# Performance work log

Hardware: AMD Instinct MI355X
Metric: run time of the kernel (lower is better)

Reference implementation:

```python
import jax, jax.numpy as jnp
import numpy as np

N_NODES = 100000
N_EDGES = 1600000
DIM = 64
N_GRAPHS = 1000


def setup_inputs() -> dict:
    key = jax.random.key(0)
    ks = jax.random.split(key, 6)
    s = 1.0 / np.sqrt(DIM)
    x = jax.random.normal(ks[0], (N_NODES, DIM), dtype=jnp.float32)
    edge_index = jax.random.randint(ks[1], (2, N_EDGES), 0, N_NODES, dtype=jnp.int64)
    batch = jnp.sort(jax.random.randint(ks[2], (N_NODES,), 0, N_GRAPHS, dtype=jnp.int64))
    W1 = jax.random.normal(ks[3], (DIM, DIM), dtype=jnp.float32) * s
    b1 = jnp.zeros((DIM,), jnp.float32)
    W2 = jax.random.normal(ks[4], (DIM, DIM), dtype=jnp.float32) * s
    b2 = jnp.zeros((DIM,), jnp.float32)
    return {"x": x, "W1": W1, "b1": b1, "W2": W2, "b2": b2,
            "edge_index": edge_index, "batch": batch}


def reference(x, W1, b1, W2, b2, edge_index, batch):
    n = x.shape[0]
    loop = jnp.arange(n, dtype=edge_index.dtype)
    src = jnp.concatenate([edge_index[0], loop])  # [E+N] with self-loops
    dst = jnp.concatenate([edge_index[1], loop])
    # symmetric GCN normalization: deg^{-1/2}[src] * deg^{-1/2}[dst]
    deg = jax.ops.segment_sum(jnp.ones(src.shape[0], x.dtype), dst, num_segments=n)
    dinv = jax.lax.rsqrt(jnp.maximum(deg, 1.0))  # deg >= 1 due to self-loops
    norm = (dinv[src] * dinv[dst])[:, None]      # [E+N, 1]

    def gcn(h, W, b):
        h = h @ W                                  # transform first (smaller dim path)
        msg = h[src] * norm                        # gather + normalize
        return jax.ops.segment_sum(msg, dst, num_segments=n) + b

    h = jax.nn.relu(gcn(x, W1, b1))
    # dropout: eval mode -> identity
    h = jax.nn.relu(gcn(h, W2, b2))

    counts = jax.ops.segment_sum(jnp.ones((n,), x.dtype), batch, num_segments=N_GRAPHS)
    pooled = jax.ops.segment_sum(h, batch, num_segments=N_GRAPHS)
    return pooled / jnp.maximum(counts, 1.0)[:, None]
```

## Files before the change

kernel.cpp:

```cpp
#include <hip/hip_runtime.h>
#include <hip/hip_fp16.h>

#define DIM 64
#define BIN_SHIFT 7
#define BINSZ 128
#define MAXBINS 1024
#define PB 512
#define PB_LOG 9

typedef __attribute__((ext_vector_type(2))) float floatx2;


__global__ __launch_bounds__(256) void k_hist(const int* __restrict__ dst,
                                              int* __restrict__ C, int E, int NB) {
    __shared__ int h[MAXBINS];
    for (int i = threadIdx.x; i < NB; i += 256) h[i] = 0;
    __syncthreads();
    int per = (E + PB - 1) / PB;
    int e0 = blockIdx.x * per;
    int e1 = e0 + per; if (e1 > E) e1 = E;
    for (int e = e0 + (int)threadIdx.x; e < e1; e += 256)
        atomicAdd(&h[dst[e] >> BIN_SHIFT], 1);
    __syncthreads();
    for (int i = threadIdx.x; i < NB; i += 256)
        C[blockIdx.x * NB + i] = h[i];
}


__global__ __launch_bounds__(1024) void k_scanA(const int* __restrict__ C,
                                                int* __restrict__ S,
                                                int* __restrict__ bsums, int NB, int M) {
    __shared__ int sh[1024];
    int tid = threadIdx.x;
    int j0 = blockIdx.x * 4096 + tid * 4;
    int v[4]; int sum = 0;
#pragma unroll
    for (int t = 0; t < 4; ++t) {
        int j = j0 + t; int x = 0;
        if (j < M) { int bin = j >> PB_LOG, blk = j & (PB - 1); x = C[blk * NB + bin]; }
        v[t] = sum; sum += x;
    }
    sh[tid] = sum;
    __syncthreads();
#pragma unroll
    for (int d = 1; d < 1024; d <<= 1) {
        int t = (tid >= d) ? sh[tid - d] : 0;
        __syncthreads();
        sh[tid] += t;
        __syncthreads();
    }
    int excl = sh[tid] - sum;
#pragma unroll
    for (int t = 0; t < 4; ++t) {
        int j = j0 + t;
        if (j < M) S[j] = excl + v[t];
    }
    if (tid == 1023) bsums[blockIdx.x] = sh[1023];
}


__global__ __launch_bounds__(1024) void k_scanB(int* __restrict__ bsums, int nb) {
    __shared__ int s[1024];
    int tid = threadIdx.x;
    int v = (tid < nb) ? bsums[tid] : 0;
    s[tid] = v;
    __syncthreads();
#pragma unroll
    for (int d = 1; d < 1024; d <<= 1) {
        int t = (tid >= d) ? s[tid - d] : 0;
        __syncthreads();
        s[tid] += t;
        __syncthreads();
    }
    if (tid < nb) bsums[tid] = s[tid] - v;
}


__global__ __launch_bounds__(256) void k_bucket(const int* __restrict__ src,
                                                const int* __restrict__ dst,
                                                const int* __restrict__ S,
                                                const int* __restrict__ bsums,
                                                int* __restrict__ bkt, int E, int NB) {
    __shared__ int lcur[MAXBINS];
    int blk = blockIdx.x;
    for (int i = threadIdx.x; i < NB; i += 256) {
        int j = i * PB + blk;
        lcur[i] = S[j] + bsums[j >> 12];
    }
    __syncthreads();
    int per = (E + PB - 1) / PB;
    int e0 = blk * per;
    int e1 = e0 + per; if (e1 > E) e1 = E;
    for (int e = e0 + (int)threadIdx.x; e < e1; e += 256) {
        int d = dst[e];
        int pos = atomicAdd(&lcur[d >> BIN_SHIFT], 1);
        bkt[pos] = src[e] | ((d & (BINSZ - 1)) << 24);
    }
}


__global__ __launch_bounds__(256) void k_binsort(const int* __restrict__ bkt,
                                                 const int* __restrict__ S,
                                                 const int* __restrict__ bsums,
                                                 int* __restrict__ csr,
                                                 int* __restrict__ off,
                                                 float* __restrict__ dinv,
                                                 const int* __restrict__ batch,
                                                 int* __restrict__ goff,
                                                 int N, int G, int E, int NB) {
    __shared__ int cnt[BINSZ], bas[BINSZ], cur[BINSZ];
    __shared__ int wsum[4];
    int tid = threadIdx.x;
    int b = blockIdx.x;
    int j0 = b << PB_LOG;
    int s0 = S[j0] + bsums[j0 >> 12];
    int s1 = E;
    if (b + 1 < NB) { int j1 = (b + 1) << PB_LOG; s1 = S[j1] + bsums[j1 >> 12]; }
    if (tid < BINSZ) { cnt[tid] = 0; cur[tid] = 0; }
    __syncthreads();
    for (int i = s0 + tid; i < s1; i += 256)
        atomicAdd(&cnt[(bkt[i] >> 24) & (BINSZ - 1)], 1);
    __syncthreads();
    int my = (tid < BINSZ) ? cnt[tid] : 0;
    int lane = tid & 63, wv = tid >> 6;
    int x = my;
#pragma unroll
    for (int d = 1; d < 64; d <<= 1) {
        int t = __shfl_up(x, d);
        if (lane >= d) x += t;
    }
    if (lane == 63) wsum[wv] = x;
    __syncthreads();
    int prefix = 0;
    for (int w = 0; w < wv; ++w) prefix += wsum[w];
    int ex = x + prefix - my;
    if (tid < BINSZ) {
        bas[tid] = ex;
        int v = (b << BIN_SHIFT) + tid;
        if (v < N) {
            off[v] = s0 + ex;
            dinv[v] = rsqrtf((float)(my + 1));
            if (v == N - 1) off[N] = E;
            int bb = batch[v];
            int prev = (v == 0) ? -1 : batch[v - 1];
            for (int g = prev + 1; g <= bb; ++g) goff[g] = v;
            if (v == N - 1)
                for (int g = bb + 1; g <= G; ++g) goff[g] = N;
        }
    }
    __syncthreads();
    for (int i = s0 + tid; i < s1; i += 256) {
        int p = bkt[i];
        int lo = (p >> 24) & (BINSZ - 1);
        int li = atomicAdd(&cur[lo], 1);
        csr[s0 + bas[lo] + li] = p & 0xFFFFFF;
    }
}


__global__ __launch_bounds__(256) void k_gemm(const float* __restrict__ Xf,
                                              const __half* __restrict__ Xh,
                                              const float* __restrict__ W,
                                              const float* __restrict__ dinv,
                                              __half* __restrict__ Y, int N,
                                              int relu_in, int fp8out) {
    __shared__ float Ws[64 * 64];
    __shared__ float Xs[16 * 64];
    int tid = threadIdx.x;
#pragma unroll
    for (int i = 0; i < 16; ++i) Ws[tid + 256 * i] = W[tid + 256 * i];

    int row0 = blockIdx.x * 16;
    int r = tid >> 4, c4 = (tid & 15) << 2;
    int row = row0 + r;
    {
        float4 v = make_float4(0.f, 0.f, 0.f, 0.f);
        if (row < N) {
            if (Xh) {
                uint2 u = *(const uint2*)(Xh + (size_t)row * DIM + c4);
                float2 f0 = __half22float2(*(__half2*)&u.x);
                float2 f1 = __half22float2(*(__half2*)&u.y);
                v = make_float4(f0.x, f0.y, f1.x, f1.y);
            } else {
                v = *(const float4*)(Xf + (size_t)row * DIM + c4);
            }
            if (relu_in) {
                v.x = fmaxf(v.x, 0.f); v.y = fmaxf(v.y, 0.f);
                v.z = fmaxf(v.z, 0.f); v.w = fmaxf(v.w, 0.f);
            }
        }
        *(float4*)(Xs + r * DIM + c4) = v;
    }
    __syncthreads();

    float4 acc = make_float4(0.f, 0.f, 0.f, 0.f);
#pragma unroll
    for (int k = 0; k < 64; ++k) {
        float xk = Xs[r * DIM + k];
        float4 w = *(const float4*)(Ws + k * DIM + c4);
        acc.x += xk * w.x; acc.y += xk * w.y;
        acc.z += xk * w.z; acc.w += xk * w.w;
    }
    if (fp8out) {
        unsigned int* Y8 = (unsigned int*)Y;
        if (row < N) {
            float s = dinv[row];
            int p = 0;
            p = __builtin_amdgcn_cvt_pk_fp8_f32(acc.x * s, acc.y * s, p, false);
            p = __builtin_amdgcn_cvt_pk_fp8_f32(acc.z * s, acc.w * s, p, true);
            Y8[(size_t)row * 16 + (c4 >> 2)] = (unsigned int)p;
        } else if (row == N) {
            Y8[(size_t)row * 16 + (c4 >> 2)] = 0u;
        }
    } else {
        if (row < N) {
            float s = dinv[row];
            __half2 p0 = __floats2half2_rn(acc.x * s, acc.y * s);
            __half2 p1 = __floats2half2_rn(acc.z * s, acc.w * s);
            uint2 u;
            u.x = *(unsigned int*)&p0;
            u.y = *(unsigned int*)&p1;
            *(uint2*)(Y + (size_t)row * DIM + c4) = u;
        } else if (row == N) {
            uint2 z; z.x = 0u; z.y = 0u;
            *(uint2*)(Y + (size_t)row * DIM + c4) = z;
        }
    }
}


__device__ __forceinline__ float4 gather_rows(const unsigned int* __restrict__ hs8,
                                              const int* __restrict__ csr,
                                              int k0, int k1, int v, int l, int gw4,
                                              int N) {
    float4 accA, accB;
    {
        unsigned int u = hs8[(size_t)v * 16 + l];
        floatx2 f0 = __builtin_amdgcn_cvt_pk_f32_fp8((int)u, false);
        floatx2 f1 = __builtin_amdgcn_cvt_pk_f32_fp8((int)u, true);
        accA = make_float4(f0.x, f0.y, f1.x, f1.y);
        accB = make_float4(0.f, 0.f, 0.f, 0.f);
    }
    for (int kb = k0; kb < k1; kb += 16) {
        int rem = k1 - kb;
        int idx = N;
        if (l < rem) idx = csr[kb + l];
        int mm = rem < 16 ? rem : 16;
        for (int j = 0; j < mm; j += 4) {
            int sA = __shfl(idx, gw4 + j);
            int sB = __shfl(idx, gw4 + j + 1);
            int sC = __shfl(idx, gw4 + j + 2);
            int sD = __shfl(idx, gw4 + j + 3);
            unsigned int uA = hs8[(size_t)sA * 16 + l];
            unsigned int uB = hs8[(size_t)sB * 16 + l];
            unsigned int uC = hs8[(size_t)sC * 16 + l];
            unsigned int uD = hs8[(size_t)sD * 16 + l];
            floatx2 pA0 = __builtin_amdgcn_cvt_pk_f32_fp8((int)uA, false);
            floatx2 pA1 = __builtin_amdgcn_cvt_pk_f32_fp8((int)uA, true);
            floatx2 pB0 = __builtin_amdgcn_cvt_pk_f32_fp8((int)uB, false);
            floatx2 pB1 = __builtin_amdgcn_cvt_pk_f32_fp8((int)uB, true);
            floatx2 pC0 = __builtin_amdgcn_cvt_pk_f32_fp8((int)uC, false);
            floatx2 pC1 = __builtin_amdgcn_cvt_pk_f32_fp8((int)uC, true);
            floatx2 pD0 = __builtin_amdgcn_cvt_pk_f32_fp8((int)uD, false);
            floatx2 pD1 = __builtin_amdgcn_cvt_pk_f32_fp8((int)uD, true);
            accA.x += pA0.x + pB0.x; accA.y += pA0.y + pB0.y;
            accA.z += pA1.x + pB1.x; accA.w += pA1.y + pB1.y;
            accB.x += pC0.x + pD0.x; accB.y += pC0.y + pD0.y;
            accB.z += pC1.x + pD1.x; accB.w += pC1.y + pD1.y;
        }
    }
    return make_float4(accA.x + accB.x, accA.y + accB.y,
                       accA.z + accB.z, accA.w + accB.w);
}


__global__ __launch_bounds__(256) void k_gather_gemm(const unsigned int* __restrict__ hs8,
                                                     const int* __restrict__ csr,
                                                     const int* __restrict__ off,
                                                     const float* __restrict__ dinv,
                                                     const float* __restrict__ bias,
                                                     const float* __restrict__ W,
                                                     unsigned int* __restrict__ hs_out,
                                                     int N) {
    __shared__ float Ws[64 * 64];
    __shared__ float Xs[16 * 64];
    int tid = threadIdx.x;
#pragma unroll
    for (int i = 0; i < 16; ++i) Ws[tid + 256 * i] = W[tid + 256 * i];
    if (blockIdx.x == 0 && tid < 16)
        hs_out[(size_t)N * 16 + tid] = 0u;

    int r = tid >> 4;
    int l = tid & 15;
    int gw4 = ((tid >> 4) & 3) << 4;
    int v = blockIdx.x * 16 + r;

    float dv = 0.f;
    float4 h = make_float4(0.f, 0.f, 0.f, 0.f);
    if (v < N) {
        dv = dinv[v];
        float4 bv = ((const float4*)bias)[l];
        float4 acc = gather_rows(hs8, csr, off[v], off[v + 1], v, l, gw4, N);
        h.x = fmaxf(acc.x * dv + bv.x, 0.f);
        h.y = fmaxf(acc.y * dv + bv.y, 0.f);
        h.z = fmaxf(acc.z * dv + bv.z, 0.f);
        h.w = fmaxf(acc.w * dv + bv.w, 0.f);
    }
    *(float4*)(Xs + r * DIM + (l << 2)) = h;
    __syncthreads();

    float4 o = make_float4(0.f, 0.f, 0.f, 0.f);
#pragma unroll
    for (int k = 0; k < 64; ++k) {
        float xk = Xs[r * DIM + k];
        float4 w = *(const float4*)(Ws + k * DIM + (l << 2));
        o.x += xk * w.x; o.y += xk * w.y;
        o.z += xk * w.z; o.w += xk * w.w;
    }
    if (v < N) {
        int p = 0;
        p = __builtin_amdgcn_cvt_pk_fp8_f32(o.x * dv, o.y * dv, p, false);
        p = __builtin_amdgcn_cvt_pk_fp8_f32(o.z * dv, o.w * dv, p, true);
        hs_out[(size_t)v * 16 + l] = (unsigned int)p;
    }
}


__global__ __launch_bounds__(256) void k_gather16(const unsigned int* __restrict__ hs8,
                                                  const int* __restrict__ csr,
                                                  const int* __restrict__ off,
                                                  const float* __restrict__ dinv,
                                                  const float* __restrict__ bias,
                                                  __half* __restrict__ agg, int N) {
    int tid = threadIdx.x;
    int v = blockIdx.x * 16 + (tid >> 4);
    if (v >= N) return;
    int l = tid & 15;
    int gw4 = ((tid >> 4) & 3) << 4;
    float dv = dinv[v];
    float4 bv = ((const float4*)bias)[l];
    float4 acc = gather_rows(hs8, csr, off[v], off[v + 1], v, l, gw4, N);
    __half2 p0 = __floats2half2_rn(acc.x * dv + bv.x, acc.y * dv + bv.y);
    __half2 p1 = __floats2half2_rn(acc.z * dv + bv.z, acc.w * dv + bv.w);
    uint2 u;
    u.x = *(unsigned int*)&p0;
    u.y = *(unsigned int*)&p1;
    ((uint2*)(agg + (size_t)v * DIM))[l] = u;
}


__global__ __launch_bounds__(256) void k_pool(const __half* __restrict__ agg,
                                              const int* __restrict__ goff,
                                              float* __restrict__ out, int G) {
    int g = blockIdx.x * 4 + (threadIdx.x >> 6);
    if (g >= G) return;
    int lane = threadIdx.x & 63;
    int q = lane >> 4, c = lane & 15;
    const uint2* h2 = (const uint2*)agg;
    int n0 = goff[g], n1 = goff[g + 1];
    float4 acc = make_float4(0.f, 0.f, 0.f, 0.f);
    for (int i = n0 + q; i < n1; i += 4) {
        uint2 u = h2[(size_t)i * 16 + c];
        float2 f0 = __half22float2(*(__half2*)&u.x);
        float2 f1 = __half22float2(*(__half2*)&u.y);
        acc.x += fmaxf(f0.x, 0.f); acc.y += fmaxf(f0.y, 0.f);
        acc.z += fmaxf(f1.x, 0.f); acc.w += fmaxf(f1.y, 0.f);
    }
    acc.x += __shfl_down(acc.x, 32); acc.y += __shfl_down(acc.y, 32);
    acc.z += __shfl_down(acc.z, 32); acc.w += __shfl_down(acc.w, 32);
    acc.x += __shfl_down(acc.x, 16); acc.y += __shfl_down(acc.y, 16);
    acc.z += __shfl_down(acc.z, 16); acc.w += __shfl_down(acc.w, 16);
    if (q == 0) {
        float inv = 1.0f / fmaxf((float)(n1 - n0), 1.0f);
        *(float4*)(out + ((size_t)g << 6) + (c << 2)) =
            make_float4(acc.x * inv, acc.y * inv, acc.z * inv, acc.w * inv);
    }
}


static inline int cdiv(int a, int b) { return (a + b - 1) / b; }

extern "C" void kernel_launch(void* const* d_in, const int* in_sizes, int n_in,
                              void* d_out, int out_size, void* d_ws, size_t ws_size,
                              hipStream_t stream) {
    const float* x   = (const float*)d_in[0];
    const float* W1  = (const float*)d_in[1];
    const float* b1  = (const float*)d_in[2];
    const float* W2  = (const float*)d_in[3];
    const float* b2  = (const float*)d_in[4];
    const int*   ei  = (const int*)d_in[5];
    const int*   bat = (const int*)d_in[6];

    const int N = in_sizes[0] / DIM;
    const int E = in_sizes[5] / 2;
    const int G = out_size / DIM;
    const int NB = cdiv(N, BINSZ);
    const int M  = NB * PB;
    const int* src = ei;
    const int* dst = ei + E;
    float* out = (float*)d_out;

    __half* hs1    = (__half*)d_ws;
    __half* hs2    = hs1 + (size_t)(N + 1) * DIM;
    __half* agg1   = hs2 + (size_t)(N + 1) * DIM;
    float*  dinv   = (float*)(agg1 + (size_t)N * DIM);
    int*    off    = (int*)(dinv + N);
    int*    goff   = off + (N + 1);
    int*    C      = goff + (G + 1);
    int*    S      = C + (size_t)PB * NB;
    int*    bsums  = S + (size_t)PB * NB;
    int*    csr    = bsums + 1024;
    int*    bkt    = (int*)hs1;
    __half* agg2   = hs1;

    k_hist<<<PB, 256, 0, stream>>>(dst, C, E, NB);
    int nb2 = cdiv(M, 4096);
    k_scanA<<<nb2, 1024, 0, stream>>>(C, S, bsums, NB, M);
    k_scanB<<<1, 1024, 0, stream>>>(bsums, nb2);
    k_bucket<<<PB, 256, 0, stream>>>(src, dst, S, bsums, bkt, E, NB);
    k_binsort<<<NB, 256, 0, stream>>>(bkt, S, bsums, csr, off, dinv, bat, goff, N, G, E, NB);

    k_gemm<<<cdiv(N + 1, 16), 256, 0, stream>>>(x, nullptr, W1, dinv, hs1, N, 0, 1);

    k_gather_gemm<<<cdiv(N, 16), 256, 0, stream>>>((const unsigned int*)hs1, csr, off,
                                                   dinv, b1, W2, (unsigned int*)hs2, N);

    k_gather16<<<cdiv(N, 16), 256, 0, stream>>>((const unsigned int*)hs2, csr, off,
                                                dinv, b2, agg2, N);

    k_pool<<<cdiv(G, 4), 256, 0, stream>>>(agg2, goff, out, G);
}
```

Before: 226.7 us.

## Sort nodes by degree within bins to balance gather waves; widen unroll

The binsort kernel now computes, within each 128-node bin, a rank of every node by in-degree and writes a permutation array. The gather kernels take their node from this permutation, so the 16-lane groups sharing a wavefront have similar edge counts and lose less time to divergence. The gather inner loop is unrolled to 8 neighbor loads with four accumulators and 32-bit index math, and the unused fp16 paths of the gemm kernel are removed. The cost is an O(128) rank loop per thread in binsort, an extra indirection per node, and scattered output writes.

```diff
diff --git a/kernel.cpp b/kernel.cpp
--- a/kernel.cpp
+++ b/kernel.cpp
@@ -107,6 +107,7 @@
                                                  float* __restrict__ dinv,
                                                  const int* __restrict__ batch,
                                                  int* __restrict__ goff,
+                                                 int* __restrict__ nperm,
                                                  int N, int G, int E, int NB) {
     __shared__ int cnt[BINSZ], bas[BINSZ], cur[BINSZ];
     __shared__ int wsum[4];
@@ -148,6 +149,21 @@
                 for (int g = bb + 1; g <= G; ++g) goff[g] = N;
         }
     }
+    if (tid < BINSZ) {
+        int v = (b << BIN_SHIFT) + tid;
+        if (v < N) {
+            int nvalid = N - (b << BIN_SHIFT);
+            if (nvalid > BINSZ) nvalid = BINSZ;
+            int d = my, rk = 0;
+            for (int j = 0; j < nvalid; ++j) {
+                int dj = cnt[j];
+                rk += (int)((dj < d) || (dj == d && j < tid));
+            }
+            nperm[(b << BIN_SHIFT) + rk] = v;
+        } else {
+            nperm[v] = N;
+        }
+    }
     __syncthreads();
     for (int i = s0 + tid; i < s1; i += 256) {
         int p = bkt[i];
@@ -159,11 +175,9 @@
 
 
 __global__ __launch_bounds__(256) void k_gemm(const float* __restrict__ Xf,
-                                              const __half* __restrict__ Xh,
                                               const float* __restrict__ W,
                                               const float* __restrict__ dinv,
-                                              __half* __restrict__ Y, int N,
-                                              int relu_in, int fp8out) {
+                                              unsigned int* __restrict__ Y8, int N) {
     __shared__ float Ws[64 * 64];
     __shared__ float Xs[16 * 64];
     int tid = threadIdx.x;
@@ -175,20 +189,7 @@
     int row = row0 + r;
     {
         float4 v = make_float4(0.f, 0.f, 0.f, 0.f);
-        if (row < N) {
-            if (Xh) {
-                uint2 u = *(const uint2*)(Xh + (size_t)row * DIM + c4);
-                float2 f0 = __half22float2(*(__half2*)&u.x);
-                float2 f1 = __half22float2(*(__half2*)&u.y);
-                v = make_float4(f0.x, f0.y, f1.x, f1.y);
-            } else {
-                v = *(const float4*)(Xf + (size_t)row * DIM + c4);
-            }
-            if (relu_in) {
-                v.x = fmaxf(v.x, 0.f); v.y = fmaxf(v.y, 0.f);
-                v.z = fmaxf(v.z, 0.f); v.w = fmaxf(v.w, 0.f);
-            }
-        }
+        if (row < N) v = *(const float4*)(Xf + (size_t)row * DIM + c4);
         *(float4*)(Xs + r * DIM + c4) = v;
     }
     __syncthreads();
@@ -201,30 +202,14 @@
         acc.x += xk * w.x; acc.y += xk * w.y;
         acc.z += xk * w.z; acc.w += xk * w.w;
     }
-    if (fp8out) {
-        unsigned int* Y8 = (unsigned int*)Y;
-        if (row < N) {
-            float s = dinv[row];
-            int p = 0;
-            p = __builtin_amdgcn_cvt_pk_fp8_f32(acc.x * s, acc.y * s, p, false);
-            p = __builtin_amdgcn_cvt_pk_fp8_f32(acc.z * s, acc.w * s, p, true);
-            Y8[(size_t)row * 16 + (c4 >> 2)] = (unsigned int)p;
-        } else if (row == N) {
-            Y8[(size_t)row * 16 + (c4 >> 2)] = 0u;
-        }
-    } else {
-        if (row < N) {
-            float s = dinv[row];
-            __half2 p0 = __floats2half2_rn(acc.x * s, acc.y * s);
-            __half2 p1 = __floats2half2_rn(acc.z * s, acc.w * s);
-            uint2 u;
-            u.x = *(unsigned int*)&p0;
-            u.y = *(unsigned int*)&p1;
-            *(uint2*)(Y + (size_t)row * DIM + c4) = u;
-        } else if (row == N) {
-            uint2 z; z.x = 0u; z.y = 0u;
-            *(uint2*)(Y + (size_t)row * DIM + c4) = z;
-        }
+    if (row < N) {
+        float s = dinv[row];
+        int p = 0;
+        p = __builtin_amdgcn_cvt_pk_fp8_f32(acc.x * s, acc.y * s, p, false);
+        p = __builtin_amdgcn_cvt_pk_fp8_f32(acc.z * s, acc.w * s, p, true);
+        Y8[(size_t)row * 16 + (c4 >> 2)] = (unsigned int)p;
+    } else if (row == N) {
+        Y8[(size_t)row * 16 + (c4 >> 2)] = 0u;
     }
 }
 
@@ -233,50 +218,74 @@
                                               const int* __restrict__ csr,
                                               int k0, int k1, int v, int l, int gw4,
                                               int N) {
-    float4 accA, accB;
+    float4 a0, a1, a2, a3;
     {
-        unsigned int u = hs8[(size_t)v * 16 + l];
+        unsigned int u = hs8[(unsigned)((v << 4) | l)];
         floatx2 f0 = __builtin_amdgcn_cvt_pk_f32_fp8((int)u, false);
         floatx2 f1 = __builtin_amdgcn_cvt_pk_f32_fp8((int)u, true);
-        accA = make_float4(f0.x, f0.y, f1.x, f1.y);
-        accB = make_float4(0.f, 0.f, 0.f, 0.f);
+        a0 = make_float4(f0.x, f0.y, f1.x, f1.y);
+        a1 = make_float4(0.f, 0.f, 0.f, 0.f);
+        a2 = make_float4(0.f, 0.f, 0.f, 0.f);
+        a3 = make_float4(0.f, 0.f, 0.f, 0.f);
     }
     for (int kb = k0; kb < k1; kb += 16) {
         int rem = k1 - kb;
-        int idx = N;
-        if (l < rem) idx = csr[kb + l];
+        int idx = (l < rem) ? csr[kb + l] : N;
         int mm = rem < 16 ? rem : 16;
-        for (int j = 0; j < mm; j += 4) {
-            int sA = __shfl(idx, gw4 + j);
-            int sB = __shfl(idx, gw4 + j + 1);
-            int sC = __shfl(idx, gw4 + j + 2);
-            int sD = __shfl(idx, gw4 + j + 3);
-            unsigned int uA = hs8[(size_t)sA * 16 + l];
-            unsigned int uB = hs8[(size_t)sB * 16 + l];
-            unsigned int uC = hs8[(size_t)sC * 16 + l];
-            unsigned int uD = hs8[(size_t)sD * 16 + l];
-            floatx2 pA0 = __builtin_amdgcn_cvt_pk_f32_fp8((int)uA, false);
-            floatx2 pA1 = __builtin_amdgcn_cvt_pk_f32_fp8((int)uA, true);
-            floatx2 pB0 = __builtin_amdgcn_cvt_pk_f32_fp8((int)uB, false);
-            floatx2 pB1 = __builtin_amdgcn_cvt_pk_f32_fp8((int)uB, true);
-            floatx2 pC0 = __builtin_amdgcn_cvt_pk_f32_fp8((int)uC, false);
-            floatx2 pC1 = __builtin_amdgcn_cvt_pk_f32_fp8((int)uC, true);
-            floatx2 pD0 = __builtin_amdgcn_cvt_pk_f32_fp8((int)uD, false);
-            floatx2 pD1 = __builtin_amdgcn_cvt_pk_f32_fp8((int)uD, true);
-            accA.x += pA0.x + pB0.x; accA.y += pA0.y + pB0.y;
-            accA.z += pA1.x + pB1.x; accA.w += pA1.y + pB1.y;
-            accB.x += pC0.x + pD0.x; accB.y += pC0.y + pD0.y;
-            accB.z += pC1.x + pD1.x; accB.w += pC1.y + pD1.y;
+        for (int j = 0; j < mm; j += 8) {
+            int s0 = __shfl(idx, gw4 + j + 0);
+            int s1 = __shfl(idx, gw4 + j + 1);
+            int s2 = __shfl(idx, gw4 + j + 2);
+            int s3 = __shfl(idx, gw4 + j + 3);
+            int s4 = __shfl(idx, gw4 + j + 4);
+            int s5 = __shfl(idx, gw4 + j + 5);
+            int s6 = __shfl(idx, gw4 + j + 6);
+            int s7 = __shfl(idx, gw4 + j + 7);
+            unsigned int u0 = hs8[(unsigned)((s0 << 4) | l)];
+            unsigned int u1 = hs8[(unsigned)((s1 << 4) | l)];
+            unsigned int u2 = hs8[(unsigned)((s2 << 4) | l)];
+            unsigned int u3 = hs8[(unsigned)((s3 << 4) | l)];
+            unsigned int u4 = hs8[(unsigned)((s4 << 4) | l)];
+            unsigned int u5 = hs8[(unsigned)((s5 << 4) | l)];
+            unsigned int u6 = hs8[(unsigned)((s6 << 4) | l)];
+            unsigned int u7 = hs8[(unsigned)((s7 << 4) | l)];
+            floatx2 p0l = __builtin_amdgcn_cvt_pk_f32_fp8((int)u0, false);
+            floatx2 p0h = __builtin_amdgcn_cvt_pk_f32_fp8((int)u0, true);
+            floatx2 p1l = __builtin_amdgcn_cvt_pk_f32_fp8((int)u1, false);
+            floatx2 p1h = __builtin_amdgcn_cvt_pk_f32_fp8((int)u1, true);
+            floatx2 p2l = __builtin_amdgcn_cvt_pk_f32_fp8((int)u2, false);
+            floatx2 p2h = __builtin_amdgcn_cvt_pk_f32_fp8((int)u2, true);
+            floatx2 p3l = __builtin_amdgcn_cvt_pk_f32_fp8((int)u3, false);
+            floatx2 p3h = __builtin_amdgcn_cvt_pk_f32_fp8((int)u3, true);
+            floatx2 p4l = __builtin_amdgcn_cvt_pk_f32_fp8((int)u4, false);
+            floatx2 p4h = __builtin_amdgcn_cvt_pk_f32_fp8((int)u4, true);
+            floatx2 p5l = __builtin_amdgcn_cvt_pk_f32_fp8((int)u5, false);
+            floatx2 p5h = __builtin_amdgcn_cvt_pk_f32_fp8((int)u5, true);
+            floatx2 p6l = __builtin_amdgcn_cvt_pk_f32_fp8((int)u6, false);
+            floatx2 p6h = __builtin_amdgcn_cvt_pk_f32_fp8((int)u6, true);
+            floatx2 p7l = __builtin_amdgcn_cvt_pk_f32_fp8((int)u7, false);
+            floatx2 p7h = __builtin_amdgcn_cvt_pk_f32_fp8((int)u7, true);
+            a0.x += p0l.x; a0.y += p0l.y; a0.z += p0h.x; a0.w += p0h.y;
+            a1.x += p1l.x; a1.y += p1l.y; a1.z += p1h.x; a1.w += p1h.y;
+            a2.x += p2l.x; a2.y += p2l.y; a2.z += p2h.x; a2.w += p2h.y;
+            a3.x += p3l.x; a3.y += p3l.y; a3.z += p3h.x; a3.w += p3h.y;
+            a0.x += p4l.x; a0.y += p4l.y; a0.z += p4h.x; a0.w += p4h.y;
+            a1.x += p5l.x; a1.y += p5l.y; a1.z += p5h.x; a1.w += p5h.y;
+            a2.x += p6l.x; a2.y += p6l.y; a2.z += p6h.x; a2.w += p6h.y;
+            a3.x += p7l.x; a3.y += p7l.y; a3.z += p7h.x; a3.w += p7h.y;
         }
     }
-    return make_float4(accA.x + accB.x, accA.y + accB.y,
-                       accA.z + accB.z, accA.w + accB.w);
+    return make_float4(a0.x + a1.x + a2.x + a3.x,
+                       a0.y + a1.y + a2.y + a3.y,
+                       a0.z + a1.z + a2.z + a3.z,
+                       a0.w + a1.w + a2.w + a3.w);
 }
 
 
 __global__ __launch_bounds__(256) void k_gather_gemm(const unsigned int* __restrict__ hs8,
                                                      const int* __restrict__ csr,
                                                      const int* __restrict__ off,
+                                                     const int* __restrict__ nperm,
                                                      const float* __restrict__ dinv,
                                                      const float* __restrict__ bias,
                                                      const float* __restrict__ W,
@@ -293,7 +302,7 @@
     int r = tid >> 4;
     int l = tid & 15;
     int gw4 = ((tid >> 4) & 3) << 4;
-    int v = blockIdx.x * 16 + r;
+    int v = nperm[blockIdx.x * 16 + r];
 
     float dv = 0.f;
     float4 h = make_float4(0.f, 0.f, 0.f, 0.f);
@@ -329,11 +338,12 @@
 __global__ __launch_bounds__(256) void k_gather16(const unsigned int* __restrict__ hs8,
                                                   const int* __restrict__ csr,
                                                   const int* __restrict__ off,
+                                                  const int* __restrict__ nperm,
                                                   const float* __restrict__ dinv,
                                                   const float* __restrict__ bias,
                                                   __half* __restrict__ agg, int N) {
     int tid = threadIdx.x;
-    int v = blockIdx.x * 16 + (tid >> 4);
+    int v = nperm[blockIdx.x * 16 + (tid >> 4)];
     if (v >= N) return;
     int l = tid & 15;
     int gw4 = ((tid >> 4) & 3) << 4;
@@ -410,6 +420,7 @@
     int*    S      = C + (size_t)PB * NB;
     int*    bsums  = S + (size_t)PB * NB;
     int*    csr    = bsums + 1024;
+    int*    nperm  = csr + E;
     int*    bkt    = (int*)hs1;
     __half* agg2   = hs1;
 
@@ -418,15 +429,18 @@
     k_scanA<<<nb2, 1024, 0, stream>>>(C, S, bsums, NB, M);
     k_scanB<<<1, 1024, 0, stream>>>(bsums, nb2);
     k_bucket<<<PB, 256, 0, stream>>>(src, dst, S, bsums, bkt, E, NB);
-    k_binsort<<<NB, 256, 0, stream>>>(bkt, S, bsums, csr, off, dinv, bat, goff, N, G, E, NB);
-
-    k_gemm<<<cdiv(N + 1, 16), 256, 0, stream>>>(x, nullptr, W1, dinv, hs1, N, 0, 1);
-
-    k_gather_gemm<<<cdiv(N, 16), 256, 0, stream>>>((const unsigned int*)hs1, csr, off,
-                                                   dinv, b1, W2, (unsigned int*)hs2, N);
-
-    k_gather16<<<cdiv(N, 16), 256, 0, stream>>>((const unsigned int*)hs2, csr, off,
-                                                dinv, b2, agg2, N);
+    k_binsort<<<NB, 256, 0, stream>>>(bkt, S, bsums, csr, off, dinv, bat, goff,
+                                      nperm, N, G, E, NB);
+
+    k_gemm<<<cdiv(N + 1, 16), 256, 0, stream>>>(x, W1, dinv, (unsigned int*)hs1, N);
+
+    const int GGRID = NB * (BINSZ / 16);
+
+    k_gather_gemm<<<GGRID, 256, 0, stream>>>((const unsigned int*)hs1, csr, off, nperm,
+                                             dinv, b1, W2, (unsigned int*)hs2, N);
+
+    k_gather16<<<GGRID, 256, 0, stream>>>((const unsigned int*)hs2, csr, off, nperm,
+                                          dinv, b2, agg2, N);
 
     k_pool<<<cdiv(G, 4), 256, 0, stream>>>(agg2, goff, out, G);
 }
```

New measurement: 232.1 us. +2.4%, slower.
